# Performance work log

Measured on AMD Instinct MI355X. Metric: run time of the kernel, lower is better.

## Reference

```python
import jax, jax.numpy as jnp
import numpy as np

# ---- module config (init kwargs) ----
EMB = 256
HIDDEN = 256
L, H, P = 4, 8, 4
CH = HIDDEN // H
PADDING_MODE = "zeros"   # 'zeros' or 'border'
ALIGN_CORNERS = False
# feature pyramid level shapes (height, width), static
SHAPES = np.array([[128, 128], [64, 64], [32, 32], [16, 16]], dtype=np.int32)
LEVEL_STARTS = np.concatenate([[0], np.cumsum(SHAPES.prod(-1))[:-1]]).astype(np.int32)

B, N = 8, 1024
I = int(SHAPES.prod(-1).sum())  # 21760


def setup_inputs() -> dict:
    key = jax.random.key(0)
    ks = jax.random.split(key, 8)
    scale = 0.02
    return {
        "img": jax.random.normal(ks[0], (B, I, EMB), jnp.float32),
        "img_shapes": jnp.asarray(SHAPES),
        "queries": jax.random.normal(ks[1], (B, N, EMB), jnp.float32),
        "reference_points": jax.random.uniform(ks[2], (B, N, 2), dtype=jnp.float32),
        "W_img": jax.random.normal(ks[3], (EMB, HIDDEN), jnp.float32) * scale,
        "b_img": jnp.zeros((HIDDEN,), jnp.float32),
        "W_q": jax.random.normal(ks[4], (EMB, H * L * P * 3), jnp.float32) * scale,
        "b_q": jnp.zeros((H * L * P * 3,), jnp.float32),
        "W_out": jax.random.normal(ks[5], (HIDDEN, EMB), jnp.float32) * scale,
        "b_out": jnp.zeros((EMB,), jnp.float32),
    }


def _msda(img, points, attn):
    """Multiscale deformable attention core.
    img:    [B, I, H, CH] flattened pyramid features
    points: [B, N, H, L, P, 2] (x, y) in [0, 1]
    attn:   [B, N, H, L, P]
    returns [B, N, H, CH]
    """
    b, _, h_, ch = img.shape
    n = points.shape[1]
    img_t = img.transpose(0, 2, 1, 3)  # [B, H, I, CH]
    levels = []
    for l in range(L):
        hh, ww = int(SHAPES[l, 0]), int(SHAPES[l, 1])
        start = int(LEVEL_STARTS[l])
        p = points[:, :, :, l]  # [B, N, H, P, 2]
        # grid_sample pixel mapping (after the module's 2*p-1 normalization)
        if ALIGN_CORNERS:
            x = p[..., 0] * (ww - 1)
            y = p[..., 1] * (hh - 1)
        else:
            x = p[..., 0] * ww - 0.5
            y = p[..., 1] * hh - 0.5
        x0 = jnp.floor(x); y0 = jnp.floor(y)
        wx = x - x0;       wy = y - y0
        x0i = x0.astype(jnp.int32); y0i = y0.astype(jnp.int32)
        acc = jnp.zeros((b, h_, n * P, ch), img.dtype)
        corners = [
            (x0i,     y0i,     (1 - wx) * (1 - wy)),
            (x0i + 1, y0i,     wx * (1 - wy)),
            (x0i,     y0i + 1, (1 - wx) * wy),
            (x0i + 1, y0i + 1, wx * wy),
        ]
        for xi, yi, cw in corners:
            if PADDING_MODE == "zeros":
                valid = (xi >= 0) & (xi < ww) & (yi >= 0) & (yi < hh)
                cw = cw * valid.astype(cw.dtype)
            xc = jnp.clip(xi, 0, ww - 1)
            yc = jnp.clip(yi, 0, hh - 1)
            idx = start + yc * ww + xc                              # [B, N, H, P]
            idx_t = idx.transpose(0, 2, 1, 3).reshape(b, h_, n * P)  # [B, H, N*P]
            g = jnp.take_along_axis(img_t, idx_t[..., None], axis=2)  # [B, H, N*P, CH]
            cw_t = cw.transpose(0, 2, 1, 3).reshape(b, h_, n * P, 1)
            acc = acc + cw_t * g
        levels.append(acc.reshape(b, h_, n, P, ch))
    samples = jnp.stack(levels, axis=3)            # [B, H, N, L, P, CH]
    attn_t = attn.transpose(0, 2, 1, 3, 4)          # [B, H, N, L, P]
    return jnp.einsum("bhnlpc,bhnlp->bnhc", samples, attn_t)


def reference(img, img_shapes, queries, reference_points, W_img, b_img, W_q, b_q, W_out, b_out):
    b, i_, _ = img.shape
    n = queries.shape[1]
    qp = (queries @ W_q + b_q).reshape(b, n, H, L, P, 3)
    offsets = qp[..., :2]                            # [B, N, H, L, P, 2]
    attn = jax.nn.softmax(qp[..., 2].reshape(b, n, H, L * P), axis=-1).reshape(b, n, H, L, P)
    img_p = (img @ W_img + b_img).reshape(b, i_, H, CH)
    shapes_f = img_shapes.astype(jnp.float32)        # [L, 2] (h, w)
    # faithful to source: offsets / img_shapes[:, None, :]
    sampling_points = reference_points[:, :, None, None, None, :] + offsets / shapes_f[:, None, :]
    out = _msda(img_p, sampling_points, attn)        # [B, N, H, CH]
    return out.reshape(b, n, HIDDEN) @ W_out + b_out
```

## Files before the change

kernel.cpp:

```cpp
#include <hip/hip_runtime.h>
#include <type_traits>
#include <utility>

#define B_    8
#define NQ_   1024
#define I_    21760
#define EMB_  256
#define HID_  256
#define H_    8
#define CH_   32

typedef float  f32x4  __attribute__((ext_vector_type(4)));
typedef __bf16 bf16x8 __attribute__((ext_vector_type(8)));
typedef short  s16x8  __attribute__((ext_vector_type(8)));

template <typename V, typename = void>
struct bf16_mfma_native : std::false_type {};
template <typename V>
struct bf16_mfma_native<V, std::void_t<decltype(__builtin_amdgcn_mfma_f32_16x16x32_bf16(
    std::declval<V>(), std::declval<V>(), std::declval<f32x4>(), 0, 0, 0))>>
    : std::true_type {};

template <typename V>
__device__ __forceinline__ f32x4 mfma_dispatch(V a, V b, f32x4 c) {
  if constexpr (bf16_mfma_native<V>::value) {
    return __builtin_amdgcn_mfma_f32_16x16x32_bf16(a, b, c, 0, 0, 0);
  } else {
    return __builtin_amdgcn_mfma_f32_16x16x32_bf16(
        __builtin_bit_cast(s16x8, a), __builtin_bit_cast(s16x8, b), c, 0, 0, 0);
  }
}

__device__ __forceinline__ f32x4 MFMA(s16x8 a, s16x8 b, f32x4 c) {
  return mfma_dispatch(__builtin_bit_cast(bf16x8, a), __builtin_bit_cast(bf16x8, b), c);
}

__device__ __forceinline__ unsigned short f2bf(float f) {
  unsigned u = __float_as_uint(f);
  u += 0x7fffu + ((u >> 16) & 1u);
  return (unsigned short)(u >> 16);
}

template <int NS, bool OUT_BF16>
__global__ __launch_bounds__(512) void gemm_k256(
    const float* __restrict__ A, const float* __restrict__ W,
    const float* __restrict__ bias, void* __restrict__ Out,
    const int N, const int Mtiles) {
  __shared__ __align__(16) short lds[32 * 264];
  const int tid  = threadIdx.x;
  const int lane = tid & 63;
  const int wave = tid >> 6;
  const int quad = lane >> 4;
  const int ln   = lane & 15;

  s16x8 bfrag[NS][8];
  float bv[NS];
#pragma unroll
  for (int st = 0; st < NS; ++st) {
    const int ng = st * 128 + wave * 16 + ln;
    bv[st] = bias[ng];
#pragma unroll
    for (int ks = 0; ks < 8; ++ks) {
      s16x8 f;
#pragma unroll
      for (int j = 0; j < 8; ++j)
        f[j] = (short)f2bf(W[(ks * 32 + quad * 8 + j) * N + ng]);
      bfrag[st][ks] = f;
    }
  }

  const int sr = tid >> 4;
  const int sc = (tid & 15) * 16;

  for (int t = blockIdx.x; t < Mtiles; t += gridDim.x) {
    const size_t rowBase = (size_t)t * 32;
    {
      const float4* src = (const float4*)(A + (rowBase + sr) * 256 + sc);
      float4 v0 = src[0], v1 = src[1], v2 = src[2], v3 = src[3];
      s16x8 p0, p1;
      p0[0] = (short)f2bf(v0.x); p0[1] = (short)f2bf(v0.y);
      p0[2] = (short)f2bf(v0.z); p0[3] = (short)f2bf(v0.w);
      p0[4] = (short)f2bf(v1.x); p0[5] = (short)f2bf(v1.y);
      p0[6] = (short)f2bf(v1.z); p0[7] = (short)f2bf(v1.w);
      p1[0] = (short)f2bf(v2.x); p1[1] = (short)f2bf(v2.y);
      p1[2] = (short)f2bf(v2.z); p1[3] = (short)f2bf(v2.w);
      p1[4] = (short)f2bf(v3.x); p1[5] = (short)f2bf(v3.y);
      p1[6] = (short)f2bf(v3.z); p1[7] = (short)f2bf(v3.w);
      *(s16x8*)&lds[sr * 264 + sc]     = p0;
      *(s16x8*)&lds[sr * 264 + sc + 8] = p1;
    }
    __syncthreads();

    f32x4 acc[NS][2];
#pragma unroll
    for (int st = 0; st < NS; ++st) {
      acc[st][0] = f32x4{bv[st], bv[st], bv[st], bv[st]};
      acc[st][1] = acc[st][0];
    }
#pragma unroll
    for (int ks = 0; ks < 8; ++ks) {
      s16x8 a0 = *(const s16x8*)&lds[ln * 264 + ks * 32 + quad * 8];
      s16x8 a1 = *(const s16x8*)&lds[(ln + 16) * 264 + ks * 32 + quad * 8];
#pragma unroll
      for (int st = 0; st < NS; ++st) {
        acc[st][0] = MFMA(a0, bfrag[st][ks], acc[st][0]);
        acc[st][1] = MFMA(a1, bfrag[st][ks], acc[st][1]);
      }
    }
#pragma unroll
    for (int st = 0; st < NS; ++st) {
      const int ng = st * 128 + wave * 16 + ln;
#pragma unroll
      for (int rt = 0; rt < 2; ++rt) {
#pragma unroll
        for (int r = 0; r < 4; ++r) {
          const size_t m = rowBase + rt * 16 + quad * 4 + r;
          if constexpr (OUT_BF16)
            ((unsigned short*)Out)[m * N + ng] = f2bf(acc[st][rt][r]);
          else
            ((float*)Out)[m * N + ng] = acc[st][rt][r];
        }
      }
    }
    __syncthreads();
  }
}

__global__ __launch_bounds__(256) void softmax_points_kernel(
    const float* __restrict__ qp, const float* __restrict__ refp,
    float* __restrict__ attn, float* __restrict__ pts) {
  const int gid = blockIdx.x * 256 + threadIdx.x;
  const int q = gid >> 3, h = gid & 7;
  const float* base = qp + (size_t)q * 384 + h * 48;

  float s[16];
  float mx = -1e30f;
#pragma unroll
  for (int lp = 0; lp < 16; ++lp) {
    s[lp] = base[lp * 3 + 2];
    mx = fmaxf(mx, s[lp]);
  }
  float sum = 0.f;
#pragma unroll
  for (int lp = 0; lp < 16; ++lp) {
    s[lp] = __expf(s[lp] - mx);
    sum += s[lp];
  }
  const float inv = 1.0f / sum;
  float* ao = attn + (size_t)gid * 16;
#pragma unroll
  for (int lp = 0; lp < 16; ++lp) ao[lp] = s[lp] * inv;

  const float rx = refp[q * 2], ry = refp[q * 2 + 1];
  float* po = pts + (size_t)gid * 32;
  const float invsh[4] = {1.f / 128.f, 1.f / 64.f, 1.f / 32.f, 1.f / 16.f};
#pragma unroll
  for (int l = 0; l < 4; ++l) {
#pragma unroll
    for (int p = 0; p < 4; ++p) {
      const int lp = l * 4 + p;
      po[lp * 2 + 0] = rx + base[lp * 3 + 0] * invsh[l];
      po[lp * 2 + 1] = ry + base[lp * 3 + 1] * invsh[l];
    }
  }
}

__global__ __launch_bounds__(128) void msda_sample_kernel(
    const unsigned int* __restrict__ imgp,
    const float* __restrict__ attn, const float* __restrict__ pts,
    float* __restrict__ out) {
  __shared__ __align__(16) float sw[128][4];
  __shared__ __align__(16) int   sib[128][4];
  const int bid = blockIdx.x;
  const int b = bid >> 10;
  const int tid = threadIdx.x;

  {
    const int h = tid >> 4, lp = tid & 15, l = lp >> 2;
    const int dims[4]   = {128, 64, 32, 16};
    const int starts[4] = {0, 16384, 20480, 21504};
    const int ww = dims[l], hh = dims[l], start = starts[l];
    const float px = pts[((size_t)bid * 8 + h) * 32 + lp * 2 + 0];
    const float py = pts[((size_t)bid * 8 + h) * 32 + lp * 2 + 1];
    const float a  = attn[((size_t)bid * 8 + h) * 16 + lp];
    const float x = px * (float)ww - 0.5f;
    const float y = py * (float)hh - 0.5f;
    const float x0f = floorf(x), y0f = floorf(y);
    const float wx = x - x0f, wy = y - y0f;
    const int x0 = (int)x0f, y0 = (int)y0f;
    const float cw[4] = {(1.f - wx) * (1.f - wy), wx * (1.f - wy),
                         (1.f - wx) * wy,          wx * wy};
#pragma unroll
    for (int c = 0; c < 4; ++c) {
      const int xi = x0 + (c & 1), yi = y0 + (c >> 1);
      const bool valid = (xi >= 0) & (xi < ww) & (yi >= 0) & (yi < hh);
      const int xc = min(max(xi, 0), ww - 1);
      const int yc = min(max(yi, 0), hh - 1);
      const int idx = start + yc * ww + xc;
      sw[tid][c]  = valid ? a * cw[c] : 0.f;
      sib[tid][c] = ((b * I_ + idx) << 7) + (h << 4);
    }
  }
  __syncthreads();

  const int h = tid >> 4, c2 = tid & 15;
  float acc0 = 0.f, acc1 = 0.f;
#pragma unroll
  for (int lp = 0; lp < 16; ++lp) {
    const float4 w4 = *(const float4*)sw[h * 16 + lp];
    const int4   i4 = *(const int4*)sib[h * 16 + lp];
    unsigned u;
    u = imgp[i4.x + c2];
    acc0 += w4.x * __uint_as_float(u << 16);
    acc1 += w4.x * __uint_as_float(u & 0xffff0000u);
    u = imgp[i4.y + c2];
    acc0 += w4.y * __uint_as_float(u << 16);
    acc1 += w4.y * __uint_as_float(u & 0xffff0000u);
    u = imgp[i4.z + c2];
    acc0 += w4.z * __uint_as_float(u << 16);
    acc1 += w4.z * __uint_as_float(u & 0xffff0000u);
    u = imgp[i4.w + c2];
    acc0 += w4.w * __uint_as_float(u << 16);
    acc1 += w4.w * __uint_as_float(u & 0xffff0000u);
  }
  float2 r;
  r.x = acc0;
  r.y = acc1;
  *(float2*)&out[(size_t)bid * 256 + h * 32 + c2 * 2] = r;
}

#define OFF_IMGP 0ULL
#define OFF_QP   89128960ULL
#define OFF_ATTN 101711872ULL
#define OFF_PTS  105906176ULL
#define OFF_MSDA 114294784ULL
#define WS_NEEDED 122683392ULL

extern "C" void kernel_launch(void* const* d_in, const int* in_sizes, int n_in,
                              void* d_out, int out_size, void* d_ws, size_t ws_size,
                              hipStream_t stream) {
  const float* img     = (const float*)d_in[0];
  const float* queries = (const float*)d_in[2];
  const float* refp    = (const float*)d_in[3];
  const float* W_img   = (const float*)d_in[4];
  const float* b_img   = (const float*)d_in[5];
  const float* W_q     = (const float*)d_in[6];
  const float* b_q     = (const float*)d_in[7];
  const float* W_out   = (const float*)d_in[8];
  const float* b_out   = (const float*)d_in[9];

  if (ws_size < WS_NEEDED) return;

  char* ws = (char*)d_ws;
  unsigned short* imgp = (unsigned short*)(ws + OFF_IMGP);
  float* qp   = (float*)(ws + OFF_QP);
  float* attn = (float*)(ws + OFF_ATTN);
  float* pts  = (float*)(ws + OFF_PTS);
  float* msda = (float*)(ws + OFF_MSDA);

  hipLaunchKernelGGL((gemm_k256<2, true>), dim3(512), dim3(512), 0, stream,
                     img, W_img, b_img, (void*)imgp, 256, I_ * B_ / 32);
  hipLaunchKernelGGL((gemm_k256<3, false>), dim3(256), dim3(512), 0, stream,
                     queries, W_q, b_q, (void*)qp, 384, B_ * NQ_ / 32);
  hipLaunchKernelGGL(softmax_points_kernel, dim3(B_ * NQ_ * H_ / 256), dim3(256), 0, stream,
                     qp, refp, attn, pts);
  hipLaunchKernelGGL(msda_sample_kernel, dim3(B_ * NQ_), dim3(128), 0, stream,
                     (const unsigned int*)imgp, attn, pts, msda);
  hipLaunchKernelGGL((gemm_k256<2, false>), dim3(256), dim3(512), 0, stream,
                     msda, W_out, b_out, d_out, 256, B_ * NQ_ / 32);
}
```

Before: 336.1 us.

## Fuse softmax into sampler, head-major image layout, paired corner loads, prefetch GEMM tiles

```diff
diff --git a/kernel.cpp b/kernel.cpp
--- a/kernel.cpp
+++ b/kernel.cpp
@@ -41,7 +41,7 @@
   return (unsigned short)(u >> 16);
 }
 
-template <int NS, bool OUT_BF16>
+template <int NS, int OUTM>
 __global__ __launch_bounds__(512) void gemm_k256(
     const float* __restrict__ A, const float* __restrict__ W,
     const float* __restrict__ bias, void* __restrict__ Out,
@@ -72,11 +72,15 @@
   const int sr = tid >> 4;
   const int sc = (tid & 15) * 16;
 
-  for (int t = blockIdx.x; t < Mtiles; t += gridDim.x) {
-    const size_t rowBase = (size_t)t * 32;
+  int t = blockIdx.x;
+  float4 v0, v1, v2, v3;
+  if (t < Mtiles) {
+    const float4* src = (const float4*)(A + ((size_t)t * 32 + sr) * 256 + sc);
+    v0 = src[0]; v1 = src[1]; v2 = src[2]; v3 = src[3];
+  }
+
+  for (; t < Mtiles; t += gridDim.x) {
     {
-      const float4* src = (const float4*)(A + (rowBase + sr) * 256 + sc);
-      float4 v0 = src[0], v1 = src[1], v2 = src[2], v3 = src[3];
       s16x8 p0, p1;
       p0[0] = (short)f2bf(v0.x); p0[1] = (short)f2bf(v0.y);
       p0[2] = (short)f2bf(v0.z); p0[3] = (short)f2bf(v0.w);
@@ -91,6 +95,14 @@
     }
     __syncthreads();
 
+    {
+      const int tn = t + gridDim.x;
+      if (tn < Mtiles) {
+        const float4* src = (const float4*)(A + ((size_t)tn * 32 + sr) * 256 + sc);
+        v0 = src[0]; v1 = src[1]; v2 = src[2]; v3 = src[3];
+      }
+    }
+
     f32x4 acc[NS][2];
 #pragma unroll
     for (int st = 0; st < NS; ++st) {
@@ -107,134 +119,134 @@
         acc[st][1] = MFMA(a1, bfrag[st][ks], acc[st][1]);
       }
     }
-#pragma unroll
-    for (int st = 0; st < NS; ++st) {
-      const int ng = st * 128 + wave * 16 + ln;
-#pragma unroll
-      for (int rt = 0; rt < 2; ++rt) {
-#pragma unroll
-        for (int r = 0; r < 4; ++r) {
-          const size_t m = rowBase + rt * 16 + quad * 4 + r;
-          if constexpr (OUT_BF16)
-            ((unsigned short*)Out)[m * N + ng] = f2bf(acc[st][rt][r]);
-          else
-            ((float*)Out)[m * N + ng] = acc[st][rt][r];
+    const size_t rowBase = (size_t)t * 32;
+    if constexpr (OUTM == 1) {
+      const int tb  = (int)(rowBase / I_);
+      const int ir0 = (int)(rowBase - (size_t)tb * I_);
+      unsigned short* O = (unsigned short*)Out;
+#pragma unroll
+      for (int st = 0; st < NS; ++st) {
+        const int ng = st * 128 + wave * 16 + ln;
+        const int hh = ng >> 5, cc = ng & 31;
+        const size_t pl = (size_t)(tb * 8 + hh) * I_;
+#pragma unroll
+        for (int rt = 0; rt < 2; ++rt) {
+#pragma unroll
+          for (int r = 0; r < 4; ++r) {
+            const size_t i = pl + (size_t)(ir0 + rt * 16 + quad * 4 + r);
+            O[i * 32 + cc] = f2bf(acc[st][rt][r]);
+          }
         }
       }
+    } else {
+      float* O = (float*)Out;
+#pragma unroll
+      for (int st = 0; st < NS; ++st) {
+        const int ng = st * 128 + wave * 16 + ln;
+#pragma unroll
+        for (int rt = 0; rt < 2; ++rt) {
+#pragma unroll
+          for (int r = 0; r < 4; ++r) {
+            const size_t m = rowBase + rt * 16 + quad * 4 + r;
+            O[m * N + ng] = acc[st][rt][r];
+          }
+        }
+      }
     }
     __syncthreads();
   }
 }
 
-__global__ __launch_bounds__(256) void softmax_points_kernel(
+__global__ __launch_bounds__(128) void msda_fused_kernel(
+    const unsigned int* __restrict__ imgp,
     const float* __restrict__ qp, const float* __restrict__ refp,
-    float* __restrict__ attn, float* __restrict__ pts) {
-  const int gid = blockIdx.x * 256 + threadIdx.x;
-  const int q = gid >> 3, h = gid & 7;
-  const float* base = qp + (size_t)q * 384 + h * 48;
-
-  float s[16];
-  float mx = -1e30f;
-#pragma unroll
-  for (int lp = 0; lp < 16; ++lp) {
-    s[lp] = base[lp * 3 + 2];
-    mx = fmaxf(mx, s[lp]);
-  }
-  float sum = 0.f;
-#pragma unroll
-  for (int lp = 0; lp < 16; ++lp) {
-    s[lp] = __expf(s[lp] - mx);
-    sum += s[lp];
-  }
-  const float inv = 1.0f / sum;
-  float* ao = attn + (size_t)gid * 16;
-#pragma unroll
-  for (int lp = 0; lp < 16; ++lp) ao[lp] = s[lp] * inv;
-
-  const float rx = refp[q * 2], ry = refp[q * 2 + 1];
-  float* po = pts + (size_t)gid * 32;
-  const float invsh[4] = {1.f / 128.f, 1.f / 64.f, 1.f / 32.f, 1.f / 16.f};
-#pragma unroll
-  for (int l = 0; l < 4; ++l) {
-#pragma unroll
-    for (int p = 0; p < 4; ++p) {
-      const int lp = l * 4 + p;
-      po[lp * 2 + 0] = rx + base[lp * 3 + 0] * invsh[l];
-      po[lp * 2 + 1] = ry + base[lp * 3 + 1] * invsh[l];
-    }
-  }
-}
-
-__global__ __launch_bounds__(128) void msda_sample_kernel(
-    const unsigned int* __restrict__ imgp,
-    const float* __restrict__ attn, const float* __restrict__ pts,
     float* __restrict__ out) {
   __shared__ __align__(16) float sw[128][4];
-  __shared__ __align__(16) int   sib[128][4];
-  const int bid = blockIdx.x;
-  const int b = bid >> 10;
+  __shared__ __align__(16) int   sib[128][2];
+  const int bid = ((blockIdx.x & 7) << 10) | (blockIdx.x >> 3);
+  const int b   = bid >> 10;
   const int tid = threadIdx.x;
 
   {
     const int h = tid >> 4, lp = tid & 15, l = lp >> 2;
-    const int dims[4]   = {128, 64, 32, 16};
-    const int starts[4] = {0, 16384, 20480, 21504};
-    const int ww = dims[l], hh = dims[l], start = starts[l];
-    const float px = pts[((size_t)bid * 8 + h) * 32 + lp * 2 + 0];
-    const float py = pts[((size_t)bid * 8 + h) * 32 + lp * 2 + 1];
-    const float a  = attn[((size_t)bid * 8 + h) * 16 + lp];
-    const float x = px * (float)ww - 0.5f;
-    const float y = py * (float)hh - 0.5f;
+    const int ww = 128 >> l;
+    const int start = (65536 - (65536 >> (2 * l))) / 3;
+    const float invsh = __uint_as_float((unsigned)(120 + l) << 23);
+
+    const float* qb = qp + (size_t)bid * 384 + h * 48 + lp * 3;
+    const float ox = qb[0], oy = qb[1], z = qb[2];
+    float m = z;
+    m = fmaxf(m, __shfl_xor(m, 1, 16));
+    m = fmaxf(m, __shfl_xor(m, 2, 16));
+    m = fmaxf(m, __shfl_xor(m, 4, 16));
+    m = fmaxf(m, __shfl_xor(m, 8, 16));
+    float e = __expf(z - m);
+    float s = e;
+    s += __shfl_xor(s, 1, 16);
+    s += __shfl_xor(s, 2, 16);
+    s += __shfl_xor(s, 4, 16);
+    s += __shfl_xor(s, 8, 16);
+    const float a = e / s;
+
+    const float rx = refp[bid * 2], ry = refp[bid * 2 + 1];
+    const float x = (rx + ox * invsh) * (float)ww - 0.5f;
+    const float y = (ry + oy * invsh) * (float)ww - 0.5f;
     const float x0f = floorf(x), y0f = floorf(y);
     const float wx = x - x0f, wy = y - y0f;
     const int x0 = (int)x0f, y0 = (int)y0f;
-    const float cw[4] = {(1.f - wx) * (1.f - wy), wx * (1.f - wy),
-                         (1.f - wx) * wy,          wx * wy};
-#pragma unroll
-    for (int c = 0; c < 4; ++c) {
-      const int xi = x0 + (c & 1), yi = y0 + (c >> 1);
-      const bool valid = (xi >= 0) & (xi < ww) & (yi >= 0) & (yi < hh);
-      const int xc = min(max(xi, 0), ww - 1);
-      const int yc = min(max(yi, 0), hh - 1);
-      const int idx = start + yc * ww + xc;
-      sw[tid][c]  = valid ? a * cw[c] : 0.f;
-      sib[tid][c] = ((b * I_ + idx) << 7) + (h << 4);
-    }
+
+    const int xb = min(max(x0, 0), ww - 2);
+    float u0 = 0.f, u1 = 0.f;
+    if (x0 >= 0 && x0 < ww)         { if (x0 == xb)     u0 += 1.f - wx; else u1 += 1.f - wx; }
+    if (x0 + 1 >= 0 && x0 + 1 < ww) { if (x0 + 1 == xb) u0 += wx;       else u1 += wx; }
+    const float wy0 = (y0 >= 0     && y0 < ww)     ? a * (1.f - wy) : 0.f;
+    const float wy1 = (y0 + 1 >= 0 && y0 + 1 < ww) ? a * wy         : 0.f;
+    const int yc0 = min(max(y0, 0), ww - 1);
+    const int yc1 = min(max(y0 + 1, 0), ww - 1);
+
+    const int pb = (b * 8 + h) * I_ + start + xb;
+    sw[tid][0] = wy0 * u0; sw[tid][1] = wy0 * u1;
+    sw[tid][2] = wy1 * u0; sw[tid][3] = wy1 * u1;
+    sib[tid][0] = (pb + yc0 * ww) * 16;
+    sib[tid][1] = (pb + yc1 * ww) * 16;
   }
   __syncthreads();
 
   const int h = tid >> 4, c2 = tid & 15;
-  float acc0 = 0.f, acc1 = 0.f;
+  const int p  = c2 >> 3;
+  const int cp = ((c2 & 7) << 1) + (p << 4);
+  float a0 = 0.f, a1 = 0.f, a2 = 0.f, a3 = 0.f;
 #pragma unroll
   for (int lp = 0; lp < 16; ++lp) {
     const float4 w4 = *(const float4*)sw[h * 16 + lp];
-    const int4   i4 = *(const int4*)sib[h * 16 + lp];
-    unsigned u;
-    u = imgp[i4.x + c2];
-    acc0 += w4.x * __uint_as_float(u << 16);
-    acc1 += w4.x * __uint_as_float(u & 0xffff0000u);
-    u = imgp[i4.y + c2];
-    acc0 += w4.y * __uint_as_float(u << 16);
-    acc1 += w4.y * __uint_as_float(u & 0xffff0000u);
-    u = imgp[i4.z + c2];
-    acc0 += w4.z * __uint_as_float(u << 16);
-    acc1 += w4.z * __uint_as_float(u & 0xffff0000u);
-    u = imgp[i4.w + c2];
-    acc0 += w4.w * __uint_as_float(u << 16);
-    acc1 += w4.w * __uint_as_float(u & 0xffff0000u);
-  }
+    const int2   ib = *(const int2*)sib[h * 16 + lp];
+    const float w0 = p ? w4.y : w4.x;
+    const float w1 = p ? w4.w : w4.z;
+    const uint2 ua = *(const uint2*)&imgp[ib.x + cp];
+    const uint2 ub = *(const uint2*)&imgp[ib.y + cp];
+    a0 += w0 * __uint_as_float(ua.x << 16);
+    a1 += w0 * __uint_as_float(ua.x & 0xffff0000u);
+    a2 += w0 * __uint_as_float(ua.y << 16);
+    a3 += w0 * __uint_as_float(ua.y & 0xffff0000u);
+    a0 += w1 * __uint_as_float(ub.x << 16);
+    a1 += w1 * __uint_as_float(ub.x & 0xffff0000u);
+    a2 += w1 * __uint_as_float(ub.y << 16);
+    a3 += w1 * __uint_as_float(ub.y & 0xffff0000u);
+  }
+  a0 += __shfl_xor(a0, 8);
+  a1 += __shfl_xor(a1, 8);
+  a2 += __shfl_xor(a2, 8);
+  a3 += __shfl_xor(a3, 8);
   float2 r;
-  r.x = acc0;
-  r.y = acc1;
-  *(float2*)&out[(size_t)bid * 256 + h * 32 + c2 * 2] = r;
+  r.x = p ? a2 : a0;
+  r.y = p ? a3 : a1;
+  *(float2*)&out[(size_t)bid * 256 + h * 32 + ((c2 & 7) << 2) + (p << 1)] = r;
 }
 
 #define OFF_IMGP 0ULL
 #define OFF_QP   89128960ULL
-#define OFF_ATTN 101711872ULL
-#define OFF_PTS  105906176ULL
-#define OFF_MSDA 114294784ULL
-#define WS_NEEDED 122683392ULL
+#define OFF_MSDA 101711872ULL
+#define WS_NEEDED 110100480ULL
 
 extern "C" void kernel_launch(void* const* d_in, const int* in_sizes, int n_in,
                               void* d_out, int out_size, void* d_ws, size_t ws_size,
@@ -254,18 +266,14 @@
   char* ws = (char*)d_ws;
   unsigned short* imgp = (unsigned short*)(ws + OFF_IMGP);
   float* qp   = (float*)(ws + OFF_QP);
-  float* attn = (float*)(ws + OFF_ATTN);
-  float* pts  = (float*)(ws + OFF_PTS);
   float* msda = (float*)(ws + OFF_MSDA);
 
-  hipLaunchKernelGGL((gemm_k256<2, true>), dim3(512), dim3(512), 0, stream,
+  hipLaunchKernelGGL((gemm_k256<2, 1>), dim3(512), dim3(512), 0, stream,
                      img, W_img, b_img, (void*)imgp, 256, I_ * B_ / 32);
-  hipLaunchKernelGGL((gemm_k256<3, false>), dim3(256), dim3(512), 0, stream,
+  hipLaunchKernelGGL((gemm_k256<3, 0>), dim3(256), dim3(512), 0, stream,
                      queries, W_q, b_q, (void*)qp, 384, B_ * NQ_ / 32);
-  hipLaunchKernelGGL(softmax_points_kernel, dim3(B_ * NQ_ * H_ / 256), dim3(256), 0, stream,
-                     qp, refp, attn, pts);
-  hipLaunchKernelGGL(msda_sample_kernel, dim3(B_ * NQ_), dim3(128), 0, stream,
-                     (const unsigned int*)imgp, attn, pts, msda);
-  hipLaunchKernelGGL((gemm_k256<2, false>), dim3(256), dim3(512), 0, stream,
+  hipLaunchKernelGGL(msda_fused_kernel, dim3(B_ * NQ_), dim3(128), 0, stream,
+                     (const unsigned int*)imgp, qp, refp, msda);
+  hipLaunchKernelGGL((gemm_k256<2, 0>), dim3(256), dim3(512), 0, stream,
                      msda, W_out, b_out, d_out, 256, B_ * NQ_ / 32);
 }
```

Result: no change. 339.7 us (+1.1%).
